# Performance work log

Hardware: AMD Instinct MI355X
Metric: run time of the kernel (lower is better)

The kernel has to match this reference:

```python
import jax, jax.numpy as jnp
import numpy as np

B, T, NE = 8, 4096, 1024
E, TOPK = 16, 2
LIN = NE + 32 + NE // 4 + NE // 4 + NE // 8 + NE // 8  # 1824
N_CITIES = 4


def setup_inputs() -> dict:
    key = jax.random.key(0)
    ks = jax.random.split(key, 11)
    s = 1.0 / np.sqrt(LIN)
    return {
        "mh_output": jax.random.normal(ks[0], (B, T, NE), jnp.float32),
        "delta_t_info": jax.random.normal(ks[1], (B, T, NE // 4), jnp.float32),
        "delta_dis_info": jax.random.normal(ks[2], (B, T, NE // 4), jnp.float32),
        "delta_rg_info": jax.random.normal(ks[3], (B, T, NE // 8), jnp.float32),
        "delta_entropy_info": jax.random.normal(ks[4], (B, T, NE // 8), jnp.float32),
        "city_embeddings": jax.random.normal(ks[5], (N_CITIES, 32), jnp.float32),
        "w_route": jax.random.uniform(ks[6], (LIN, E), jnp.float32, -s, s),
        "b_route": jax.random.uniform(ks[7], (E,), jnp.float32, -s, s),
        "w_noise": jax.random.uniform(ks[8], (LIN, E), jnp.float32, -s, s),
        "b_noise": jax.random.uniform(ks[9], (E,), jnp.float32, -s, s),
        "noise_eps": jax.random.normal(ks[10], (B, T, E), jnp.float32),
        "city_index": 0,
    }


def reference(mh_output, delta_t_info, delta_dis_info, delta_rg_info,
              delta_entropy_info, city_embeddings, w_route, b_route,
              w_noise, b_noise, noise_eps, city_index):
    b, t, _ = mh_output.shape
    city_embed = city_embeddings[city_index]  # [32]
    city_embeds = jnp.broadcast_to(city_embed[None, None, :], (b, t, 32))
    x = jnp.concatenate([mh_output, city_embeds, delta_t_info, delta_dis_info,
                         delta_rg_info, delta_entropy_info], axis=-1)  # [B,T,LIN]
    logits = jnp.einsum('btf,fe->bte', x, w_route) + b_route
    noise_logits = jnp.einsum('btf,fe->bte', x, w_noise) + b_noise
    noisy_logits = logits + noise_eps * jax.nn.softplus(noise_logits)  # training path
    gate1 = jax.nn.softmax(noisy_logits, axis=-1)
    top_k_logits, indices = jax.lax.top_k(noisy_logits, TOPK)  # [B,T,K]
    # scatter top-k values into a -inf tensor == mask non-topk entries to -inf
    mask = jnp.sum(jax.nn.one_hot(indices, noisy_logits.shape[-1], dtype=jnp.bool_), axis=-2) > 0
    sparse_logits = jnp.where(mask, noisy_logits, -jnp.inf)
    router_output = jax.nn.softmax(sparse_logits, axis=-1)
    return router_output, indices, gate1
```

## Files before the change

### kernel.cpp

```cpp
#include <hip/hip_runtime.h>
#include <math.h>


#define TOKS 32
#define NCHUNK 28
#define I_OFF 524288
#define G_OFF 589824

#define SA_STRIDE 68
#define SW_STRIDE 36
#define SS_STRIDE 132

__device__ __forceinline__ float softplus_f(float x) {
  return fmaxf(x, 0.0f) + log1pf(expf(-fabsf(x)));
}

__device__ __forceinline__ float get_comp(const float4& v, int kk) {
  return kk == 0 ? v.x : kk == 1 ? v.y : kk == 2 ? v.z : v.w;
}

__global__ __launch_bounds__(256, 4) void router_kernel(
    const float* __restrict__ mh, const float* __restrict__ dt,
    const float* __restrict__ dd, const float* __restrict__ rg,
    const float* __restrict__ de, const float* __restrict__ cemb_all,
    const float* __restrict__ w_route, const float* __restrict__ b_route,
    const float* __restrict__ w_noise, const float* __restrict__ b_noise,
    const float* __restrict__ eps, const int* __restrict__ city_index,
    float* __restrict__ out) {
  __shared__ float smem[4480];
  __shared__ float city_l[32];
  float* sA = smem;
  float* sW = smem + 2176;
  float* sS = smem;

  const int tid = threadIdx.x;
  const int w   = tid >> 6;
  const int ln  = tid & 63;
  const int tg  = ln & 7;
  const int eg  = ln >> 3;
  const int blockTok = blockIdx.x * TOKS;

  const int ar0 = tid >> 4,        ac0 = (tid & 15) * 4;
  const int ar1 = (tid + 256) >> 4, ac1 = (tid & 15) * 4;
  const int wr0 = tid >> 3,        wc0 = tid & 7;
  const int wr1 = (tid + 256) >> 3, wc1 = tid & 7;

  if (tid < 32) {
    const int e = tid & 15;
    const float* wsrc = (tid < 16) ? w_route : w_noise;
    const float* bsrc = (tid < 16) ? b_route : b_noise;
    const float* ce = cemb_all + city_index[0] * 32;
    float s = bsrc[e];
#pragma unroll
    for (int j = 0; j < 32; ++j) s = fmaf(ce[j], wsrc[(1024 + j) * 16 + e], s);
    city_l[tid] = s;
  }

  float4 acc0 = make_float4(0.f,0.f,0.f,0.f);
  float4 acc1 = make_float4(0.f,0.f,0.f,0.f);
  float4 acc2 = make_float4(0.f,0.f,0.f,0.f);
  float4 acc3 = make_float4(0.f,0.f,0.f,0.f);

  float4 Areg0, Areg1, Wreg0, Wreg1;

  auto a_src = [&](int g, int row) -> const float* {
    const float* base; int stride;
    if (g < 16)      { base = mh + g * 64;        stride = 1024; }
    else if (g < 20) { base = dt + (g - 16) * 64; stride = 256; }
    else if (g < 24) { base = dd + (g - 20) * 64; stride = 256; }
    else if (g < 26) { base = rg + (g - 24) * 64; stride = 128; }
    else             { base = de + (g - 26) * 64; stride = 128; }
    return base + (size_t)(blockTok + row) * stride;
  };

  auto prefetch = [&](int g) {
    Areg0 = *(const float4*)(a_src(g, ar0) + ac0);
    Areg1 = *(const float4*)(a_src(g, ar1) + ac1);
    const int kb = g * 64 + ((g * 64 >= 1024) ? 32 : 0);
    const float* s0 = (wc0 < 4) ? (w_route + (kb + wr0) * 16 + wc0 * 4)
                                : (w_noise + (kb + wr0) * 16 + (wc0 - 4) * 4);
    const float* s1 = (wc1 < 4) ? (w_route + (kb + wr1) * 16 + wc1 * 4)
                                : (w_noise + (kb + wr1) * 16 + (wc1 - 4) * 4);
    Wreg0 = *(const float4*)s0;
    Wreg1 = *(const float4*)s1;
  };

  prefetch(0);

  for (int c = 0; c < NCHUNK; ++c) {
    __syncthreads();
    *(float4*)&sA[ar0 * SA_STRIDE + ac0] = Areg0;
    *(float4*)&sA[ar1 * SA_STRIDE + ac1] = Areg1;
    *(float4*)&sW[wr0 * SW_STRIDE + wc0 * 4] = Wreg0;
    *(float4*)&sW[wr1 * SW_STRIDE + wc1 * 4] = Wreg1;
    __syncthreads();

    if (c + 1 < NCHUNK) prefetch(c + 1);

#pragma unroll
    for (int qq = 0; qq < 4; ++qq) {
      const int koff = w * 16 + qq * 4;
      float4 a0 = *(const float4*)&sA[(tg +  0) * SA_STRIDE + koff];
      float4 a1 = *(const float4*)&sA[(tg +  8) * SA_STRIDE + koff];
      float4 a2 = *(const float4*)&sA[(tg + 16) * SA_STRIDE + koff];
      float4 a3 = *(const float4*)&sA[(tg + 24) * SA_STRIDE + koff];
#pragma unroll
      for (int kk = 0; kk < 4; ++kk) {
        float4 wv = *(const float4*)&sW[(koff + kk) * SW_STRIDE + eg * 4];
        float s;
        s = get_comp(a0, kk);
        acc0.x = fmaf(s, wv.x, acc0.x); acc0.y = fmaf(s, wv.y, acc0.y);
        acc0.z = fmaf(s, wv.z, acc0.z); acc0.w = fmaf(s, wv.w, acc0.w);
        s = get_comp(a1, kk);
        acc1.x = fmaf(s, wv.x, acc1.x); acc1.y = fmaf(s, wv.y, acc1.y);
        acc1.z = fmaf(s, wv.z, acc1.z); acc1.w = fmaf(s, wv.w, acc1.w);
        s = get_comp(a2, kk);
        acc2.x = fmaf(s, wv.x, acc2.x); acc2.y = fmaf(s, wv.y, acc2.y);
        acc2.z = fmaf(s, wv.z, acc2.z); acc2.w = fmaf(s, wv.w, acc2.w);
        s = get_comp(a3, kk);
        acc3.x = fmaf(s, wv.x, acc3.x); acc3.y = fmaf(s, wv.y, acc3.y);
        acc3.z = fmaf(s, wv.z, acc3.z); acc3.w = fmaf(s, wv.w, acc3.w);
      }
    }
  }

  __syncthreads();
  {
    float* s0 = &sS[(tg +  0) * SS_STRIDE + w * 32 + eg * 4];
    float* s1 = &sS[(tg +  8) * SS_STRIDE + w * 32 + eg * 4];
    float* s2 = &sS[(tg + 16) * SS_STRIDE + w * 32 + eg * 4];
    float* s3 = &sS[(tg + 24) * SS_STRIDE + w * 32 + eg * 4];
    *(float4*)s0 = acc0; *(float4*)s1 = acc1;
    *(float4*)s2 = acc2; *(float4*)s3 = acc3;
  }
  __syncthreads();

  if (tid < TOKS) {
    const int tokg = blockTok + tid;
    float l[32];
#pragma unroll
    for (int e4 = 0; e4 < 8; ++e4) {
      float4 s0 = *(const float4*)&sS[tid * SS_STRIDE +  0 + e4 * 4];
      float4 s1 = *(const float4*)&sS[tid * SS_STRIDE + 32 + e4 * 4];
      float4 s2 = *(const float4*)&sS[tid * SS_STRIDE + 64 + e4 * 4];
      float4 s3 = *(const float4*)&sS[tid * SS_STRIDE + 96 + e4 * 4];
      l[e4 * 4 + 0] = s0.x + s1.x + s2.x + s3.x + city_l[e4 * 4 + 0];
      l[e4 * 4 + 1] = s0.y + s1.y + s2.y + s3.y + city_l[e4 * 4 + 1];
      l[e4 * 4 + 2] = s0.z + s1.z + s2.z + s3.z + city_l[e4 * 4 + 2];
      l[e4 * 4 + 3] = s0.w + s1.w + s2.w + s3.w + city_l[e4 * 4 + 3];
    }

    const float* ep = eps + (size_t)tokg * 16;
    float n[16];
#pragma unroll
    for (int e = 0; e < 16; ++e)
      n[e] = fmaf(ep[e], softplus_f(l[16 + e]), l[e]);

    float m1 = -INFINITY; int i1 = 0;
#pragma unroll
    for (int e = 0; e < 16; ++e)
      if (n[e] > m1) { m1 = n[e]; i1 = e; }
    float m2 = -INFINITY; int i2 = 0;
#pragma unroll
    for (int e = 0; e < 16; ++e)
      if (e != i1 && n[e] > m2) { m2 = n[e]; i2 = e; }

    float ex[16], Z = 0.f;
#pragma unroll
    for (int e = 0; e < 16; ++e) { ex[e] = expf(n[e] - m1); Z += ex[e]; }
    const float invZ  = 1.0f / Z;
    const float invZ2 = 1.0f / (1.0f + expf(m2 - m1));

    float r[16], g1[16];
#pragma unroll
    for (int e = 0; e < 16; ++e) {
      r[e]  = (e == i1 || e == i2) ? ex[e] * invZ2 : 0.0f;
      g1[e] = ex[e] * invZ;
    }

    float* ro = out + (size_t)tokg * 16;
#pragma unroll
    for (int e4 = 0; e4 < 4; ++e4)
      *(float4*)(ro + e4 * 4) = make_float4(r[e4*4], r[e4*4+1], r[e4*4+2], r[e4*4+3]);

    out[I_OFF + (size_t)tokg * 2 + 0] = (float)i1;
    out[I_OFF + (size_t)tokg * 2 + 1] = (float)i2;

    float* go = out + G_OFF + (size_t)tokg * 16;
#pragma unroll
    for (int e4 = 0; e4 < 4; ++e4)
      *(float4*)(go + e4 * 4) = make_float4(g1[e4*4], g1[e4*4+1], g1[e4*4+2], g1[e4*4+3]);
  }
}

extern "C" void kernel_launch(void* const* d_in, const int* in_sizes, int n_in,
                              void* d_out, int out_size, void* d_ws, size_t ws_size,
                              hipStream_t stream) {
  const float* mh = (const float*)d_in[0];
  const float* dt = (const float*)d_in[1];
  const float* dd = (const float*)d_in[2];
  const float* rg = (const float*)d_in[3];
  const float* de = (const float*)d_in[4];
  const float* ce = (const float*)d_in[5];
  const float* wr = (const float*)d_in[6];
  const float* br = (const float*)d_in[7];
  const float* wn = (const float*)d_in[8];
  const float* bn = (const float*)d_in[9];
  const float* ep = (const float*)d_in[10];
  const int*   ci = (const int*)d_in[11];
  float* out = (float*)d_out;

  router_kernel<<<1024, 256, 0, stream>>>(mh, dt, dd, rg, de, ce, wr, br, wn, bn,
                                          ep, ci, out);
}
```

Baseline: 304.2 us.

## Give each lane one token with all 32 experts, read weights via scalar loads

```diff
diff --git a/kernel.cpp b/kernel.cpp
--- a/kernel.cpp
+++ b/kernel.cpp
@@ -2,13 +2,11 @@
 #include <math.h>
 
 
-#define TOKS 32
+#define TOKS 64
 #define NCHUNK 28
 #define I_OFF 524288
 #define G_OFF 589824
-
 #define SA_STRIDE 68
-#define SW_STRIDE 36
 #define SS_STRIDE 132
 
 __device__ __forceinline__ float softplus_f(float x) {
@@ -19,7 +17,7 @@
   return kk == 0 ? v.x : kk == 1 ? v.y : kk == 2 ? v.z : v.w;
 }
 
-__global__ __launch_bounds__(256, 4) void router_kernel(
+__global__ __launch_bounds__(256, 2) void router_kernel(
     const float* __restrict__ mh, const float* __restrict__ dt,
     const float* __restrict__ dd, const float* __restrict__ rg,
     const float* __restrict__ de, const float* __restrict__ cemb_all,
@@ -27,23 +25,16 @@
     const float* __restrict__ w_noise, const float* __restrict__ b_noise,
     const float* __restrict__ eps, const int* __restrict__ city_index,
     float* __restrict__ out) {
-  __shared__ float smem[4480];
+  __shared__ float smem[8448];
   __shared__ float city_l[32];
   float* sA = smem;
-  float* sW = smem + 2176;
   float* sS = smem;
 
   const int tid = threadIdx.x;
+  const int ln  = tid & 63;
   const int w   = tid >> 6;
-  const int ln  = tid & 63;
-  const int tg  = ln & 7;
-  const int eg  = ln >> 3;
+  const int wu  = __builtin_amdgcn_readfirstlane(w);
   const int blockTok = blockIdx.x * TOKS;
-
-  const int ar0 = tid >> 4,        ac0 = (tid & 15) * 4;
-  const int ar1 = (tid + 256) >> 4, ac1 = (tid & 15) * 4;
-  const int wr0 = tid >> 3,        wc0 = tid & 7;
-  const int wr1 = (tid + 256) >> 3, wc1 = tid & 7;
 
   if (tid < 32) {
     const int e = tid & 15;
@@ -56,12 +47,14 @@
     city_l[tid] = s;
   }
 
-  float4 acc0 = make_float4(0.f,0.f,0.f,0.f);
-  float4 acc1 = make_float4(0.f,0.f,0.f,0.f);
-  float4 acc2 = make_float4(0.f,0.f,0.f,0.f);
-  float4 acc3 = make_float4(0.f,0.f,0.f,0.f);
+  float acc[32];
+#pragma unroll
+  for (int e = 0; e < 32; ++e) acc[e] = 0.0f;
 
-  float4 Areg0, Areg1, Wreg0, Wreg1;
+  const int acol = (tid & 15) * 4;
+  const int arow = tid >> 4;
+
+  float4 AR0, AR1, AR2, AR3;
 
   auto a_src = [&](int g, int row) -> const float* {
     const float* base; int stride;
@@ -74,65 +67,48 @@
   };
 
   auto prefetch = [&](int g) {
-    Areg0 = *(const float4*)(a_src(g, ar0) + ac0);
-    Areg1 = *(const float4*)(a_src(g, ar1) + ac1);
-    const int kb = g * 64 + ((g * 64 >= 1024) ? 32 : 0);
-    const float* s0 = (wc0 < 4) ? (w_route + (kb + wr0) * 16 + wc0 * 4)
-                                : (w_noise + (kb + wr0) * 16 + (wc0 - 4) * 4);
-    const float* s1 = (wc1 < 4) ? (w_route + (kb + wr1) * 16 + wc1 * 4)
-                                : (w_noise + (kb + wr1) * 16 + (wc1 - 4) * 4);
-    Wreg0 = *(const float4*)s0;
-    Wreg1 = *(const float4*)s1;
+    AR0 = *(const float4*)(a_src(g, arow +  0) + acol);
+    AR1 = *(const float4*)(a_src(g, arow + 16) + acol);
+    AR2 = *(const float4*)(a_src(g, arow + 32) + acol);
+    AR3 = *(const float4*)(a_src(g, arow + 48) + acol);
   };
 
   prefetch(0);
 
   for (int c = 0; c < NCHUNK; ++c) {
     __syncthreads();
-    *(float4*)&sA[ar0 * SA_STRIDE + ac0] = Areg0;
-    *(float4*)&sA[ar1 * SA_STRIDE + ac1] = Areg1;
-    *(float4*)&sW[wr0 * SW_STRIDE + wc0 * 4] = Wreg0;
-    *(float4*)&sW[wr1 * SW_STRIDE + wc1 * 4] = Wreg1;
+    *(float4*)&sA[(arow +  0) * SA_STRIDE + acol] = AR0;
+    *(float4*)&sA[(arow + 16) * SA_STRIDE + acol] = AR1;
+    *(float4*)&sA[(arow + 32) * SA_STRIDE + acol] = AR2;
+    *(float4*)&sA[(arow + 48) * SA_STRIDE + acol] = AR3;
     __syncthreads();
 
     if (c + 1 < NCHUNK) prefetch(c + 1);
 
+    const int kb = c * 64 + wu * 16 + ((c >= 16) ? 32 : 0);
+
 #pragma unroll
-    for (int qq = 0; qq < 4; ++qq) {
-      const int koff = w * 16 + qq * 4;
-      float4 a0 = *(const float4*)&sA[(tg +  0) * SA_STRIDE + koff];
-      float4 a1 = *(const float4*)&sA[(tg +  8) * SA_STRIDE + koff];
-      float4 a2 = *(const float4*)&sA[(tg + 16) * SA_STRIDE + koff];
-      float4 a3 = *(const float4*)&sA[(tg + 24) * SA_STRIDE + koff];
+    for (int q = 0; q < 4; ++q) {
+      float4 a = *(const float4*)&sA[ln * SA_STRIDE + wu * 16 + q * 4];
 #pragma unroll
       for (int kk = 0; kk < 4; ++kk) {
-        float4 wv = *(const float4*)&sW[(koff + kk) * SW_STRIDE + eg * 4];
-        float s;
-        s = get_comp(a0, kk);
-        acc0.x = fmaf(s, wv.x, acc0.x); acc0.y = fmaf(s, wv.y, acc0.y);
-        acc0.z = fmaf(s, wv.z, acc0.z); acc0.w = fmaf(s, wv.w, acc0.w);
-        s = get_comp(a1, kk);
-        acc1.x = fmaf(s, wv.x, acc1.x); acc1.y = fmaf(s, wv.y, acc1.y);
-        acc1.z = fmaf(s, wv.z, acc1.z); acc1.w = fmaf(s, wv.w, acc1.w);
-        s = get_comp(a2, kk);
-        acc2.x = fmaf(s, wv.x, acc2.x); acc2.y = fmaf(s, wv.y, acc2.y);
-        acc2.z = fmaf(s, wv.z, acc2.z); acc2.w = fmaf(s, wv.w, acc2.w);
-        s = get_comp(a3, kk);
-        acc3.x = fmaf(s, wv.x, acc3.x); acc3.y = fmaf(s, wv.y, acc3.y);
-        acc3.z = fmaf(s, wv.z, acc3.z); acc3.w = fmaf(s, wv.w, acc3.w);
+        const int krow = kb + q * 4 + kk;
+        const float* Wr = w_route + krow * 16;
+        const float* Wn = w_noise + krow * 16;
+        const float av = get_comp(a, kk);
+#pragma unroll
+        for (int e = 0; e < 16; ++e) acc[e]      = fmaf(av, Wr[e], acc[e]);
+#pragma unroll
+        for (int e = 0; e < 16; ++e) acc[16 + e] = fmaf(av, Wn[e], acc[16 + e]);
       }
     }
   }
 
   __syncthreads();
-  {
-    float* s0 = &sS[(tg +  0) * SS_STRIDE + w * 32 + eg * 4];
-    float* s1 = &sS[(tg +  8) * SS_STRIDE + w * 32 + eg * 4];
-    float* s2 = &sS[(tg + 16) * SS_STRIDE + w * 32 + eg * 4];
-    float* s3 = &sS[(tg + 24) * SS_STRIDE + w * 32 + eg * 4];
-    *(float4*)s0 = acc0; *(float4*)s1 = acc1;
-    *(float4*)s2 = acc2; *(float4*)s3 = acc3;
-  }
+#pragma unroll
+  for (int e4 = 0; e4 < 8; ++e4)
+    *(float4*)&sS[ln * SS_STRIDE + w * 32 + e4 * 4] =
+        make_float4(acc[e4 * 4], acc[e4 * 4 + 1], acc[e4 * 4 + 2], acc[e4 * 4 + 3]);
   __syncthreads();
 
   if (tid < TOKS) {
@@ -210,6 +186,6 @@
   const int*   ci = (const int*)d_in[11];
   float* out = (float*)d_out;
 
-  router_kernel<<<1024, 256, 0, stream>>>(mh, dt, dd, rg, de, ce, wr, br, wn, bn,
-                                          ep, ci, out);
+  router_kernel<<<512, 256, 0, stream>>>(mh, dt, dd, rg, de, ce, wr, br, wn, bn,
+                                         ep, ci, out);
 }
```

Result: slower. 386.6 us (+27.1%).
